# Optimization experiments

Hardware: AMD Instinct MI355X
Metric: run time of the kernel (lower is better)

Reference implementation:

```python
import jax, jax.numpy as jnp
import numpy as np

NUM_ROT = 8
OUT_CH = 128
IN_CH = 128
KSIZE = 3


def _resample(filt, angle):
    """Rotate a (O, I, k, k) filter bank by `angle` via bilinear resampling,
    matching F.affine_grid/F.grid_sample with align_corners=True, zero padding."""
    k = filt.shape[-1]
    c, s = jnp.cos(angle), jnp.sin(angle)
    lin = jnp.linspace(-1.0, 1.0, k)
    gy, gx = jnp.meshgrid(lin, lin, indexing='ij')  # (k, k) output coords
    # theta = [[c, -s, 0], [s, c, 0]] applied to (x, y, 1)
    xs = c * gx - s * gy
    ys = s * gx + c * gy
    ix = (xs + 1.0) * 0.5 * (k - 1)  # normalized -> pixel coords
    iy = (ys + 1.0) * 0.5 * (k - 1)
    x0f, y0f = jnp.floor(ix), jnp.floor(iy)
    x0, y0 = x0f.astype(jnp.int32), y0f.astype(jnp.int32)
    wx, wy = ix - x0f, iy - y0f

    def tap(yi, xi, w):
        valid = ((yi >= 0) & (yi < k) & (xi >= 0) & (xi < k)).astype(filt.dtype)
        yc = jnp.clip(yi, 0, k - 1)
        xc = jnp.clip(xi, 0, k - 1)
        return filt[:, :, yc, xc] * (valid * w)  # (O, I, k, k)

    return (tap(y0, x0, (1 - wy) * (1 - wx)) + tap(y0, x0 + 1, (1 - wy) * wx)
            + tap(y0 + 1, x0, wy * (1 - wx)) + tap(y0 + 1, x0 + 1, wy * wx))


def setup_inputs() -> dict:
    key = jax.random.key(0)
    k1, k2, k3 = jax.random.split(key, 3)
    x = jax.random.normal(k1, (16, IN_CH, 128, 128), jnp.float32)
    # base_conv.weight: (out_channels * num_rotations, in_channels, k, k)
    weight = jax.random.normal(k2, (OUT_CH * NUM_ROT, IN_CH, KSIZE, KSIZE), jnp.float32) * 0.05
    rot_alpha = jax.random.normal(k3, (NUM_ROT,), jnp.float32) * 0.1 + 1.0
    return {"x": x, "weight": weight, "rot_alpha": rot_alpha}


def reference(x, weight, rot_alpha):
    R, O, K = NUM_ROT, OUT_CH, KSIZE
    # weight.view(O, R, I, K, K)[:, i] per rotation -> (R, O, I, K, K)
    w_r = weight.reshape(O, R, -1, K, K).transpose(1, 0, 2, 3, 4)
    angles = rot_alpha * (jnp.pi / 4) * jnp.arange(R, dtype=jnp.float32)
    rot_w = jax.vmap(_resample)(w_r, angles)  # (R, O, I, K, K)
    filters = rot_w.reshape(R * O, -1, K, K)
    # one conv with all rotated filter banks instead of R separate convs
    y = jax.lax.conv_general_dilated(
        x, filters, window_strides=(1, 1),
        padding=[(K // 2, K // 2), (K // 2, K // 2)],
        dimension_numbers=('NCHW', 'OIHW', 'NCHW'))  # (B, R*O, H, W)
    B, _, H, W = y.shape
    return y.reshape(B, R, O, H, W).max(axis=1)  # max over rotations
```

## Files before the change

### kernel.cpp

```cpp
#include <hip/hip_runtime.h>

typedef short short8 __attribute__((ext_vector_type(8)));
typedef float f32x4 __attribute__((ext_vector_type(4)));

#define XP_BYTES (16ull * 130 * 130 * 128 * 2)

static __device__ __forceinline__ unsigned short f2bf(float f) {
  unsigned u = __float_as_uint(f);
  u += 0x7FFFu + ((u >> 16) & 1u);
  return (unsigned short)(u >> 16);
}

static __device__ __forceinline__ void gload16(const void* g, void* l) {
  __builtin_amdgcn_global_load_lds(
      (const __attribute__((address_space(1))) void*)g,
      (__attribute__((address_space(3))) void*)l, 16, 0, 0);
}

static __device__ __forceinline__ float wtap(const float* f, int yi, int xi) {
  bool valid = (yi >= 0) & (yi < 3) & (xi >= 0) & (xi < 3);
  int yc = min(max(yi, 0), 2), xc = min(max(xi, 0), 2);
  return valid ? f[yc * 3 + xc] : 0.f;
}

__global__ __launch_bounds__(256) void wprep_kernel(
    const float* __restrict__ w, const float* __restrict__ rot_alpha,
    unsigned short* __restrict__ w2) {
  int gid = blockIdx.x * 256 + threadIdx.x;
  int ic = gid & 127;
  int nr = gid >> 7;
  int r = nr & 7;
  const float* wf = w + (size_t)nr * (128 * 9) + (size_t)ic * 9;
  float f[9];
#pragma unroll
  for (int q = 0; q < 9; ++q) f[q] = wf[q];
  float ang = rot_alpha[r] * 0.78539816339744830962f * (float)r;
  float sth, cth;
  sincosf(ang, &sth, &cth);
#pragma unroll
  for (int j = 0; j < 3; ++j) {
#pragma unroll
    for (int i = 0; i < 3; ++i) {
      float gy = (float)(j - 1), gx = (float)(i - 1);
      float xs = cth * gx - sth * gy;
      float ys = sth * gx + cth * gy;
      float ix = xs + 1.0f, iy = ys + 1.0f;
      float x0f = floorf(ix), y0f = floorf(iy);
      int x0 = (int)x0f, y0 = (int)y0f;
      float wx = ix - x0f, wy = iy - y0f;
      float acc = wtap(f, y0, x0) * (1.f - wy) * (1.f - wx)
                + wtap(f, y0, x0 + 1) * (1.f - wy) * wx
                + wtap(f, y0 + 1, x0) * wy * (1.f - wx)
                + wtap(f, y0 + 1, x0 + 1) * wy * wx;
      w2[(size_t)nr * 1152 + (size_t)(j * 3 + i) * 128 + ic] = f2bf(acc);
    }
  }
}

__global__ __launch_bounds__(256) void xprep_kernel(
    const float* __restrict__ x, unsigned short* __restrict__ xp) {
  const int yy = blockIdx.x;
  const int b = blockIdx.y;
  const int t = threadIdx.x;
  const size_t rowbase = ((size_t)b * 130 + yy) * (130 * 128);
  if (yy == 0 || yy == 129) {
    uint4 z = {0u, 0u, 0u, 0u};
    for (int i = t; i < 2080; i += 256)
      ((uint4*)(xp + rowbase))[i] = z;
    return;
  }
  const int y = yy - 1;
  __shared__ float lt[32][129];
  if (t < 32) {
    uint4 z = {0u, 0u, 0u, 0u};
    int xx = (t < 16) ? 0 : 129;
    int cc = (t & 15) * 8;
    *(uint4*)(xp + rowbase + (size_t)xx * 128 + cc) = z;
  }
  for (int c0 = 0; c0 < 128; c0 += 32) {
#pragma unroll
    for (int i = 0; i < 16; ++i) {
      int idx = i * 256 + t;
      int c = idx >> 7, wq = idx & 127;
      lt[c][wq] = x[(((size_t)b * 128 + c0 + c) * 128 + y) * 128 + wq];
    }
    __syncthreads();
#pragma unroll
    for (int i = 0; i < 2; ++i) {
      int u = i * 256 + t;
      int xx = u >> 2, cp = (u & 3) * 8;
      unsigned short v[8];
#pragma unroll
      for (int q = 0; q < 8; ++q) v[q] = f2bf(lt[cp + q][xx]);
      *(uint4*)(xp + rowbase + (size_t)(xx + 1) * 128 + c0 + cp) = *(uint4*)v;
    }
    __syncthreads();
  }
}

__global__ __launch_bounds__(256, 4) void conv_kernel(
    const unsigned short* __restrict__ xp,
    const unsigned short* __restrict__ w2,
    float* __restrict__ out) {
  __shared__ unsigned short lds[16384];

  const int tid = threadIdx.x;
  const int lane = tid & 63;
  const int wv = tid >> 6;
  const int wr = wv >> 1;
  const int wc = wv & 1;

  const int bid = blockIdx.x;
  const int wg = (bid & 7) * 2048 + (bid >> 3);
  const int mblk = wg >> 3;
  const int nblk = wg & 7;
  const int b = mblk >> 7;
  const int y = mblk & 127;

  const int r0 = tid >> 2;
  const int s0 = tid & 3;
  const int g0 = s0 ^ ((r0 >> 1) & 3);

  const unsigned short* xpt =
      xp + (size_t)(b * 130 + y) * 130 * 128 + r0 * 128 + g0 * 8;
  const unsigned short* wpt =
      w2 + (size_t)nblk * 128 * 1152 + (size_t)r0 * 1152 + g0 * 8;

  const int l15 = lane & 15;
  const int lhi = lane >> 4;
  const int sa = (lhi ^ ((l15 >> 1) & 3)) * 8;
  const int aRd = wr * 2048 + l15 * 32 + sa;
  const int bRd = 8192 + wc * 2048 + l15 * 32 + sa;

  f32x4 acc[4][4];
#pragma unroll
  for (int mf = 0; mf < 4; ++mf)
#pragma unroll
    for (int nf = 0; nf < 4; ++nf) acc[mf][nf] = (f32x4){0.f, 0.f, 0.f, 0.f};

#define STAGE_T(P, T)                                                         \
  {                                                                           \
    const int tp_ = (T) >> 2, cq_ = (T) & 3;                                  \
    const int dy_ = tp_ / 3, dx_ = tp_ - dy_ * 3;                             \
    _Pragma("unroll") for (int hf_ = 0; hf_ < 2; ++hf_) {                     \
      gload16(xpt + ((size_t)dy_ * 130 + hf_ * 64 + dx_) * 128 + cq_ * 32,    \
              lds + (P) * 4096 + hf_ * 2048 + wv * 512);                      \
      gload16(wpt + (size_t)hf_ * 64 * 1152 + tp_ * 128 + cq_ * 32,           \
              lds + 8192 + (P) * 4096 + hf_ * 2048 + wv * 512);               \
    }                                                                         \
  }

#define VMW0 asm volatile("s_waitcnt vmcnt(0)" ::: "memory")
#define SCH0 __builtin_amdgcn_sched_barrier(0)

#define BODY(P, T)                                                            \
  {                                                                           \
    if ((T) + 1 < 36) STAGE_T((P) ^ 1, (T) + 1);                              \
    const unsigned short* pA_ = lds + (P) * 4096 + aRd;                       \
    const unsigned short* pB_ = lds + (P) * 4096 + bRd;                       \
    short8 af[4], bf[4];                                                      \
    _Pragma("unroll") for (int q = 0; q < 4; ++q)                             \
        af[q] = *(const short8*)(pA_ + q * 512);                              \
    _Pragma("unroll") for (int n = 0; n < 4; ++n)                             \
        bf[n] = *(const short8*)(pB_ + n * 512);                              \
    __builtin_amdgcn_s_setprio(1);                                            \
    _Pragma("unroll") for (int q = 0; q < 4; ++q)                             \
        _Pragma("unroll") for (int n = 0; n < 4; ++n)                         \
            acc[q][n] = __builtin_amdgcn_mfma_f32_16x16x32_bf16(              \
                af[q], bf[n], acc[q][n], 0, 0, 0);                            \
    __builtin_amdgcn_s_setprio(0);                                            \
    SCH0;                                                                     \
    VMW0;                                                                     \
    __builtin_amdgcn_s_barrier();                                             \
  }

  STAGE_T(0, 0);
  VMW0;
  SCH0;
  __builtin_amdgcn_s_barrier();

#pragma unroll 1
  for (int j = 0; j < 18; ++j) {
    BODY(0, 2 * j);
    BODY(1, 2 * j + 1);
  }

#undef BODY
#undef STAGE_T
#undef VMW0
#undef SCH0

  float* lE = (float*)lds;
#pragma unroll
  for (int mf = 0; mf < 4; ++mf)
#pragma unroll
    for (int nf = 0; nf < 4; ++nf)
#pragma unroll
      for (int j = 0; j < 4; ++j) {
        float v = acc[mf][nf][j];
        v = fmaxf(v, __shfl_xor(v, 1, 64));
        v = fmaxf(v, __shfl_xor(v, 2, 64));
        v = fmaxf(v, __shfl_xor(v, 4, 64));
        if ((lane & 7) == 0) {
          int pix = wr * 64 + mf * 16 + lhi * 4 + j;
          int ol = wc * 8 + nf * 2 + ((lane >> 3) & 1);
          lE[pix * 17 + ol] = v;
        }
      }
  __syncthreads();
  const size_t obase = ((size_t)(b * 128 + nblk * 16) * 128 + y) * 128;
#pragma unroll
  for (int i = 0; i < 8; ++i) {
    int idx = i * 256 + tid;
    int ol = idx >> 7;
    int xx = idx & 127;
    out[obase + (size_t)ol * 16384 + xx] = lE[xx * 17 + ol];
  }
}

extern "C" void kernel_launch(void* const* d_in, const int* in_sizes, int n_in,
                              void* d_out, int out_size, void* d_ws, size_t ws_size,
                              hipStream_t stream) {
  const float* x = (const float*)d_in[0];
  const float* w = (const float*)d_in[1];
  const float* ra = (const float*)d_in[2];
  float* out = (float*)d_out;
  unsigned short* xp = (unsigned short*)d_ws;
  unsigned short* w2 = (unsigned short*)((char*)d_ws + XP_BYTES);

  hipLaunchKernelGGL(wprep_kernel, dim3(512), dim3(256), 0, stream, w, ra, w2);
  hipLaunchKernelGGL(xprep_kernel, dim3(130, 16), dim3(256), 0, stream, x, xp);
  hipLaunchKernelGGL(conv_kernel, dim3(16384), dim3(256), 0, stream, xp, w2, out);
}
```

Before: 731.4 us.

## Reuse staged input row strip across the three horizontal filter taps

```diff
diff --git a/kernel.cpp b/kernel.cpp
--- a/kernel.cpp
+++ b/kernel.cpp
@@ -102,7 +102,7 @@
     const unsigned short* __restrict__ xp,
     const unsigned short* __restrict__ w2,
     float* __restrict__ out) {
-  __shared__ unsigned short lds[16384];
+  __shared__ unsigned short lds[16640];
 
   const int tid = threadIdx.x;
   const int lane = tid & 63;
@@ -128,9 +128,10 @@
 
   const int l15 = lane & 15;
   const int lhi = lane >> 4;
-  const int sa = (lhi ^ ((l15 >> 1) & 3)) * 8;
-  const int aRd = wr * 2048 + l15 * 32 + sa;
-  const int bRd = 8192 + wc * 2048 + l15 * 32 + sa;
+  const int aRd0 = wr * 2048 + (l15 + 0) * 32 + ((lhi ^ (((l15 + 0) >> 1) & 3)) * 8);
+  const int aRd1 = wr * 2048 + (l15 + 1) * 32 + ((lhi ^ (((l15 + 1) >> 1) & 3)) * 8);
+  const int aRd2 = wr * 2048 + (l15 + 2) * 32 + ((lhi ^ (((l15 + 2) >> 1) & 3)) * 8);
+  const int bRd = wc * 2048 + l15 * 32 + ((lhi ^ ((l15 >> 1) & 3)) * 8);
 
   f32x4 acc[4][4];
 #pragma unroll
@@ -138,26 +139,36 @@
 #pragma unroll
     for (int nf = 0; nf < 4; ++nf) acc[mf][nf] = (f32x4){0.f, 0.f, 0.f, 0.f};
 
-#define STAGE_T(P, T)                                                         \
+#define STAGE_A_STRIP(BUFA, S)                                                \
   {                                                                           \
-    const int tp_ = (T) >> 2, cq_ = (T) & 3;                                  \
-    const int dy_ = tp_ / 3, dx_ = tp_ - dy_ * 3;                             \
-    _Pragma("unroll") for (int hf_ = 0; hf_ < 2; ++hf_) {                     \
-      gload16(xpt + ((size_t)dy_ * 130 + hf_ * 64 + dx_) * 128 + cq_ * 32,    \
-              lds + (P) * 4096 + hf_ * 2048 + wv * 512);                      \
-      gload16(wpt + (size_t)hf_ * 64 * 1152 + tp_ * 128 + cq_ * 32,           \
-              lds + 8192 + (P) * 4096 + hf_ * 2048 + wv * 512);               \
+    const int dy_ = (S) % 3, cq_ = (S) / 3;                                   \
+    const unsigned short* src_ = xpt + (size_t)dy_ * 130 * 128 + cq_ * 32;    \
+    gload16(src_, lds + (BUFA) * 4224 + wv * 512);                            \
+    gload16(src_ + 64 * 128, lds + (BUFA) * 4224 + 2048 + wv * 512);          \
+    if (tid < 8) {                                                            \
+      const unsigned short* ts_ =                                             \
+          xp + ((size_t)(b * 130 + y + dy_)) * 130 * 128 +                    \
+          (size_t)(128 + (tid >> 2)) * 128 + cq_ * 32 + (tid & 3) * 8;        \
+      gload16(ts_, lds + (BUFA) * 4224 + 4096);                               \
     }                                                                         \
+  }
+
+#define STAGE_B_T(BUFB, TAP, CQ)                                              \
+  {                                                                           \
+    gload16(wpt + (TAP) * 128 + (CQ) * 32,                                    \
+            lds + 8448 + (BUFB) * 4096 + wv * 512);                           \
+    gload16(wpt + (size_t)64 * 1152 + (TAP) * 128 + (CQ) * 32,                \
+            lds + 8448 + (BUFB) * 4096 + 2048 + wv * 512);                    \
   }
 
 #define VMW0 asm volatile("s_waitcnt vmcnt(0)" ::: "memory")
 #define SCH0 __builtin_amdgcn_sched_barrier(0)
 
-#define BODY(P, T)                                                            \
+#define BODY(BUFA, BUFB, ARD, STG)                                            \
   {                                                                           \
-    if ((T) + 1 < 36) STAGE_T((P) ^ 1, (T) + 1);                              \
-    const unsigned short* pA_ = lds + (P) * 4096 + aRd;                       \
-    const unsigned short* pB_ = lds + (P) * 4096 + bRd;                       \
+    STG;                                                                      \
+    const unsigned short* pA_ = lds + (BUFA) * 4224 + (ARD);                  \
+    const unsigned short* pB_ = lds + 8448 + (BUFB) * 4096 + bRd;             \
     short8 af[4], bf[4];                                                      \
     _Pragma("unroll") for (int q = 0; q < 4; ++q)                             \
         af[q] = *(const short8*)(pA_ + q * 512);                              \
@@ -174,19 +185,38 @@
     __builtin_amdgcn_s_barrier();                                             \
   }
 
-  STAGE_T(0, 0);
+  STAGE_A_STRIP(0, 0);
+  STAGE_B_T(0, 0, 0);
   VMW0;
   SCH0;
   __builtin_amdgcn_s_barrier();
 
 #pragma unroll 1
-  for (int j = 0; j < 18; ++j) {
-    BODY(0, 2 * j);
-    BODY(1, 2 * j + 1);
+  for (int j = 0; j < 6; ++j) {
+    {
+      const int s_ = 2 * j;
+      const int dy_ = s_ % 3, cq_ = s_ / 3;
+      const int tap_ = dy_ * 3;
+      const int dyn_ = (s_ + 1) % 3, cqn_ = (s_ + 1) / 3;
+      BODY(0, 0, aRd0, STAGE_B_T(1, tap_ + 1, cq_));
+      BODY(0, 1, aRd1, { STAGE_A_STRIP(1, s_ + 1); STAGE_B_T(0, tap_ + 2, cq_); });
+      BODY(0, 0, aRd2, STAGE_B_T(1, dyn_ * 3, cqn_));
+    }
+    {
+      const int s_ = 2 * j + 1;
+      const int dy_ = s_ % 3, cq_ = s_ / 3;
+      const int tap_ = dy_ * 3;
+      const bool more_ = s_ < 11;
+      const int dyn_ = (s_ + 1) % 3, cqn_ = (s_ + 1) / 3;
+      BODY(1, 1, aRd0, STAGE_B_T(0, tap_ + 1, cq_));
+      BODY(1, 0, aRd1, { if (more_) STAGE_A_STRIP(0, s_ + 1); STAGE_B_T(1, tap_ + 2, cq_); });
+      BODY(1, 1, aRd2, { if (more_) STAGE_B_T(0, dyn_ * 3, cqn_); });
+    }
   }
 
 #undef BODY
-#undef STAGE_T
+#undef STAGE_A_STRIP
+#undef STAGE_B_T
 #undef VMW0
 #undef SCH0
 
```

Result: slower. 925.6 us (+26.6%).

## Give each wave private LDS tiles and drop per-step workgroup barriers

Applied to the files above, without the earlier changes.

```diff
diff --git a/kernel.cpp b/kernel.cpp
--- a/kernel.cpp
+++ b/kernel.cpp
@@ -98,11 +98,11 @@
   }
 }
 
-__global__ __launch_bounds__(256, 4) void conv_kernel(
+__global__ __launch_bounds__(256, 2) void conv_kernel(
     const unsigned short* __restrict__ xp,
     const unsigned short* __restrict__ w2,
     float* __restrict__ out) {
-  __shared__ unsigned short lds[16384];
+  __shared__ unsigned short lds[32768];
 
   const int tid = threadIdx.x;
   const int lane = tid & 63;
@@ -117,20 +117,17 @@
   const int b = mblk >> 7;
   const int y = mblk & 127;
 
-  const int r0 = tid >> 2;
-  const int s0 = tid & 3;
-  const int g0 = s0 ^ ((r0 >> 1) & 3);
-
-  const unsigned short* xpt =
-      xp + (size_t)(b * 130 + y) * 130 * 128 + r0 * 128 + g0 * 8;
-  const unsigned short* wpt =
-      w2 + (size_t)nblk * 128 * 1152 + (size_t)r0 * 1152 + g0 * 8;
+  const int gsl = (lane & 3) ^ ((lane >> 3) & 3);
+  const unsigned short* xw =
+      xp + ((size_t)(b * 130 + y)) * 130 * 128 +
+      (size_t)(wr * 64 + (lane >> 2)) * 128 + gsl * 8;
+  const unsigned short* wB =
+      w2 + (size_t)(nblk * 128 + wc * 64 + (lane >> 2)) * 1152 + gsl * 8;
 
   const int l15 = lane & 15;
   const int lhi = lane >> 4;
-  const int sa = (lhi ^ ((l15 >> 1) & 3)) * 8;
-  const int aRd = wr * 2048 + l15 * 32 + sa;
-  const int bRd = 8192 + wc * 2048 + l15 * 32 + sa;
+  const int aRd = l15 * 32 + ((lhi ^ ((l15 >> 1) & 3)) * 8);
+  unsigned short* const myl = lds + wv * 4096;
 
   f32x4 acc[4][4];
 #pragma unroll
@@ -142,22 +139,27 @@
   {                                                                           \
     const int tp_ = (T) >> 2, cq_ = (T) & 3;                                  \
     const int dy_ = tp_ / 3, dx_ = tp_ - dy_ * 3;                             \
-    _Pragma("unroll") for (int hf_ = 0; hf_ < 2; ++hf_) {                     \
-      gload16(xpt + ((size_t)dy_ * 130 + hf_ * 64 + dx_) * 128 + cq_ * 32,    \
-              lds + (P) * 4096 + hf_ * 2048 + wv * 512);                      \
-      gload16(wpt + (size_t)hf_ * 64 * 1152 + tp_ * 128 + cq_ * 32,           \
-              lds + 8192 + (P) * 4096 + hf_ * 2048 + wv * 512);               \
-    }                                                                         \
-  }
-
+    const unsigned short* sa_ = xw + (size_t)(dy_ * 130 + dx_) * 128 + cq_ * 32; \
+    const unsigned short* sb_ = wB + tp_ * 128 + cq_ * 32;                    \
+    _Pragma("unroll") for (int i_ = 0; i_ < 4; ++i_)                          \
+        gload16(sa_ + (size_t)i_ * 16 * 128, myl + (P) * 16384 + i_ * 512);   \
+    _Pragma("unroll") for (int i_ = 0; i_ < 4; ++i_)                          \
+        gload16(sb_ + (size_t)i_ * 16 * 1152,                                 \
+                myl + (P) * 16384 + 2048 + i_ * 512);                         \
+  }
+
+#define VMW8 asm volatile("s_waitcnt vmcnt(8)" ::: "memory")
 #define VMW0 asm volatile("s_waitcnt vmcnt(0)" ::: "memory")
 #define SCH0 __builtin_amdgcn_sched_barrier(0)
 
 #define BODY(P, T)                                                            \
   {                                                                           \
-    if ((T) + 1 < 36) STAGE_T((P) ^ 1, (T) + 1);                              \
-    const unsigned short* pA_ = lds + (P) * 4096 + aRd;                       \
-    const unsigned short* pB_ = lds + (P) * 4096 + bRd;                       \
+    SCH0;                                                                     \
+    if ((T) + 1 < 36) { STAGE_T((P) ^ 1, (T) + 1); VMW8; }                    \
+    else { VMW0; }                                                            \
+    SCH0;                                                                     \
+    const unsigned short* pA_ = myl + (P) * 16384 + aRd;                      \
+    const unsigned short* pB_ = myl + (P) * 16384 + 2048 + aRd;               \
     short8 af[4], bf[4];                                                      \
     _Pragma("unroll") for (int q = 0; q < 4; ++q)                             \
         af[q] = *(const short8*)(pA_ + q * 512);                              \
@@ -169,15 +171,9 @@
             acc[q][n] = __builtin_amdgcn_mfma_f32_16x16x32_bf16(              \
                 af[q], bf[n], acc[q][n], 0, 0, 0);                            \
     __builtin_amdgcn_s_setprio(0);                                            \
-    SCH0;                                                                     \
-    VMW0;                                                                     \
-    __builtin_amdgcn_s_barrier();                                             \
   }
 
   STAGE_T(0, 0);
-  VMW0;
-  SCH0;
-  __builtin_amdgcn_s_barrier();
 
 #pragma unroll 1
   for (int j = 0; j < 18; ++j) {
@@ -187,9 +183,11 @@
 
 #undef BODY
 #undef STAGE_T
+#undef VMW8
 #undef VMW0
 #undef SCH0
 
+  __syncthreads();
   float* lE = (float*)lds;
 #pragma unroll
   for (int mf = 0; mf < 4; ++mf)
```

After: 962.9 us. 1.32x slower.
